# Kernel optimization log

Measured on AMD Instinct MI355X. Metric: run time of the kernel, lower is better.

Reference implementation:

```python
import jax, jax.numpy as jnp
import numpy as np

PI_APPROX = 3.1415926  # the source uses 3.1415926, not math.pi
N_RINGS = 10
N_ANGLES = 36  # k in range(0, 360, 10)


def setup_inputs() -> dict:
    key = jax.random.key(0)
    k1, k2, k3 = jax.random.split(key, 3)
    B, N = 32, 16384
    pred = jax.random.normal(k1, (B, N_RINGS), dtype=jnp.float32)
    target = jax.random.normal(k2, (B, N, 3), dtype=jnp.float32)
    trans_feat = jax.random.normal(k3, (B, 256), dtype=jnp.float32)
    return {"pred": pred, "target": target, "trans_feat": trans_feat}


def _generate_points(pred):
    # pred: [B, 10] radii. For ring j: center = [0.04, 0.15*j - 0.7, 0.0],
    # axis = y, firstPoint (centered) = [-r, 0, 0]. Rotating about y by angle a:
    # R @ [-r,0,0] = [-r*cos(a), 0, r*sin(a)]; then add center back.
    B = pred.shape[0]
    j = jnp.arange(N_RINGS, dtype=pred.dtype)
    cy = 0.15 * j - 0.7                                   # [10]
    ang = jnp.arange(0, 360, 10, dtype=pred.dtype) * (2.0 * PI_APPROX / 360.0)  # [36]
    c, s = jnp.cos(ang), jnp.sin(ang)
    r = pred[:, :, None]                                  # [B,10,1]
    px = -r * c[None, None, :] + 0.04                     # [B,10,36]
    py = jnp.broadcast_to(cy[None, :, None], px.shape)    # [B,10,36]
    pz = r * s[None, None, :]                             # [B,10,36]
    pts = jnp.stack([px, py, pz], axis=-1)                # [B,10,36,3]
    return pts.reshape(B, N_RINGS * N_ANGLES, 3)          # [B,360,3]


def reference(pred, target, trans_feat):
    B = pred.shape[0]
    pts = _generate_points(pred.reshape(B, N_RINGS))      # [B,360,3]
    # squared pairwise distances via ||a||^2 + ||b||^2 - 2 a.b
    d2 = (jnp.sum(pts * pts, axis=-1)[:, :, None]
          + jnp.sum(target * target, axis=-1)[:, None, :]
          - 2.0 * jnp.einsum('bpd,bnd->bpn', pts, target))  # [B,360,N]
    d2 = jnp.maximum(d2, 0.0)
    # original: min over target of ||pt - tgt||, then squared == min of squared dist
    min_d2 = jnp.min(d2, axis=-1)                         # [B,360]
    return jnp.mean(min_d2)
```

## Files before the change

kernel.cpp:

```cpp
#include <hip/hip_runtime.h>
#include <math.h>
#include <float.h>

#define N_RINGS  10
#define N_ANGLES 36
#define NP       (N_RINGS * N_ANGLES)
#define PI_APPROX 3.1415926f

#define BLOCK  256
#define WPB    4
#define CHUNK  1024
#define NPAIR  (CHUNK / 2)
#define PPT    6

typedef float f2 __attribute__((ext_vector_type(2)));

__global__ __launch_bounds__(BLOCK) void chamfer_minbuf(
    const float* __restrict__ pred,
    const float* __restrict__ target,
    unsigned int* __restrict__ minbuf,
    int N, int chunks)
{
    __shared__ float4 txy[NPAIR];
    __shared__ float4 tzw[NPAIR];
    __shared__ float  pm[WPB * NP];
    __shared__ float  cs_c[N_ANGLES], cs_s[N_ANGLES];

    const int b   = blockIdx.x / chunks;
    const int cg  = blockIdx.x % chunks;
    const int n0  = cg * CHUNK;
    const int tid = threadIdx.x;
    const int cnt = min(CHUNK, N - n0);
    const int npairs = (cnt + 1) >> 1;

    if (tid < N_ANGLES) {
        float angf = (float)(10 * tid) * (2.0f * PI_APPROX / 360.0f);
        double ang = (double)angf;
        cs_c[tid] = (float)cos(ang);
        cs_s[tid] = (float)sin(ang);
    }
    for (int p = tid; p < npairs; p += BLOCK) {
        const int i0 = 2 * p;
        const int i1 = min(2 * p + 1, cnt - 1);
        const float* t0 = target + ((size_t)b * N + (size_t)(n0 + i0)) * 3;
        const float* t1 = target + ((size_t)b * N + (size_t)(n0 + i1)) * 3;
        float x0 = t0[0], y0 = t0[1], z0 = t0[2];
        float x1 = t1[0], y1 = t1[1], z1 = t1[2];
        float w0 = x0 * x0 + y0 * y0 + z0 * z0;
        float w1 = x1 * x1 + y1 * y1 + z1 * z1;
        txy[p] = make_float4(x0, x1, y0, y1);
        tzw[p] = make_float4(z0, z1, w0, w1);
    }
    __syncthreads();

    const int lane = tid & 63;
    const int w    = tid >> 6;

    f2 qx2[PPT], qy2[PPT], qz2[PPT], m2[PPT];
    float pp2[PPT];
    #pragma unroll
    for (int k = 0; k < PPT; ++k) {
        int s = lane + 64 * k;
        int j = s / N_ANGLES;
        int a = s - j * N_ANGLES;
        int jc = (j < N_RINGS) ? j : (N_RINGS - 1);
        float r  = pred[b * N_RINGS + jc];
        float px = -r * cs_c[a] + 0.04f;
        float py = 0.15f * (float)jc - 0.7f;
        float pz = r * cs_s[a];
        pp2[k] = px * px + py * py + pz * pz;
        float qxv = -2.0f * px, qyv = -2.0f * py, qzv = -2.0f * pz;
        qx2[k] = (f2){qxv, qxv};
        qy2[k] = (f2){qyv, qyv};
        qz2[k] = (f2){qzv, qzv};
        m2[k]  = (f2){FLT_MAX, FLT_MAX};
    }

    #pragma unroll 4
    for (int k = w; k < npairs; k += WPB) {
        float4 A  = txy[k];
        float4 Bz = tzw[k];
        f2 X  = {A.x,  A.y };
        f2 Y  = {A.z,  A.w };
        f2 Z  = {Bz.x, Bz.y};
        f2 W2 = {Bz.z, Bz.w};
        #pragma unroll
        for (int i = 0; i < PPT; ++i) {
            f2 h = __builtin_elementwise_fma(qz2[i], Z, W2);
            h = __builtin_elementwise_fma(qy2[i], Y, h);
            h = __builtin_elementwise_fma(qx2[i], X, h);
            m2[i] = __builtin_elementwise_min(m2[i], h);
        }
    }

    #pragma unroll
    for (int k = 0; k < PPT; ++k) {
        int s = lane + 64 * k;
        if (s < NP) {
            float mv = fminf(m2[k].x, m2[k].y);
            pm[w * NP + s] = fmaxf(pp2[k] + mv, 0.0f);
        }
    }
    __syncthreads();

    for (int p = tid; p < NP; p += BLOCK) {
        float v = fminf(fminf(pm[p], pm[NP + p]),
                        fminf(pm[2 * NP + p], pm[3 * NP + p]));
        atomicMin(&minbuf[b * NP + p], __float_as_uint(v));
    }
}

__global__ __launch_bounds__(1024) void reduce_mean(
    const unsigned int* __restrict__ minbuf, float* __restrict__ out,
    int count)
{
    __shared__ double sm[16];
    const int tid = threadIdx.x;
    double s = 0.0;
    const int n4 = count >> 2;
    const uint4* v4 = (const uint4*)minbuf;
    for (int i = tid; i < n4; i += 1024) {
        uint4 u = v4[i];
        s += (double)__uint_as_float(u.x) + (double)__uint_as_float(u.y)
           + (double)__uint_as_float(u.z) + (double)__uint_as_float(u.w);
    }
    for (int i = 4 * n4 + tid; i < count; i += 1024)
        s += (double)__uint_as_float(minbuf[i]);
    #pragma unroll
    for (int off = 32; off > 0; off >>= 1)
        s += __shfl_down(s, off, 64);
    if ((tid & 63) == 0) sm[tid >> 6] = s;
    __syncthreads();
    if (tid == 0) {
        double tot = 0.0;
        for (int wv = 0; wv < 16; ++wv) tot += sm[wv];
        out[0] = (float)(tot / (double)count);
    }
}

extern "C" void kernel_launch(void* const* d_in, const int* in_sizes, int n_in,
                              void* d_out, int out_size, void* d_ws, size_t ws_size,
                              hipStream_t stream) {
    const float* pred   = (const float*)d_in[0];
    const float* target = (const float*)d_in[1];

    const int B = in_sizes[0] / N_RINGS;
    const int N = in_sizes[1] / (3 * B);
    const int chunks = (N + CHUNK - 1) / CHUNK;
    const int count  = B * NP;

    unsigned int* minbuf = (unsigned int*)d_ws;
    float* out = (float*)d_out;

    hipMemsetAsync(minbuf, 0xFF, (size_t)count * sizeof(unsigned int), stream);

    hipLaunchKernelGGL(chamfer_minbuf, dim3(B * chunks), dim3(BLOCK), 0, stream,
                       pred, target, minbuf, N, chunks);
    hipLaunchKernelGGL(reduce_mean, dim3(1), dim3(1024), 0, stream,
                       minbuf, out, count);
}
```

Baseline: 81.45 us.

## Fuse mean reduction into chamfer kernel via last-block ticket and double block size

Removes the separate single-block reduce kernel by having each block take a ticket from an atomic counter placed after the min buffer. The last block to finish sums the min buffer and writes the mean. The counter is initialised to 0xFFFFFFFF by the memset, which is why the last block is detected as gridDim-2. The block size also grows to 512 threads with 8 waves splitting the target chunk, which cuts per-wave loop length but adds an 8-way min merge. This saves a kernel launch at the cost of a fence and atomic in every block, plus a serial tail done by a 512-thread block.

```diff
diff --git a/kernel.cpp b/kernel.cpp
--- a/kernel.cpp
+++ b/kernel.cpp
@@ -7,24 +7,27 @@
 #define NP       (N_RINGS * N_ANGLES)
 #define PI_APPROX 3.1415926f
 
-#define BLOCK  256
-#define WPB    4
+#define BLOCK  512
+#define WPB    8
 #define CHUNK  1024
 #define NPAIR  (CHUNK / 2)
 #define PPT    6
 
 typedef float f2 __attribute__((ext_vector_type(2)));
 
-__global__ __launch_bounds__(BLOCK) void chamfer_minbuf(
+__global__ __launch_bounds__(BLOCK, 4) void chamfer_fused(
     const float* __restrict__ pred,
     const float* __restrict__ target,
     unsigned int* __restrict__ minbuf,
-    int N, int chunks)
+    float* __restrict__ out,
+    int N, int chunks, int count)
 {
     __shared__ float4 txy[NPAIR];
     __shared__ float4 tzw[NPAIR];
     __shared__ float  pm[WPB * NP];
     __shared__ float  cs_c[N_ANGLES], cs_s[N_ANGLES];
+    __shared__ unsigned int ticket;
+    __shared__ double sm[WPB];
 
     const int b   = blockIdx.x / chunks;
     const int cg  = blockIdx.x % chunks;
@@ -104,37 +107,36 @@
     __syncthreads();
 
     for (int p = tid; p < NP; p += BLOCK) {
-        float v = fminf(fminf(pm[p], pm[NP + p]),
-                        fminf(pm[2 * NP + p], pm[3 * NP + p]));
+        float v = pm[p];
+        #pragma unroll
+        for (int wv = 1; wv < WPB; ++wv)
+            v = fminf(v, pm[wv * NP + p]);
         atomicMin(&minbuf[b * NP + p], __float_as_uint(v));
     }
-}
 
-__global__ __launch_bounds__(1024) void reduce_mean(
-    const unsigned int* __restrict__ minbuf, float* __restrict__ out,
-    int count)
-{
-    __shared__ double sm[16];
-    const int tid = threadIdx.x;
-    double s = 0.0;
-    const int n4 = count >> 2;
-    const uint4* v4 = (const uint4*)minbuf;
-    for (int i = tid; i < n4; i += 1024) {
-        uint4 u = v4[i];
-        s += (double)__uint_as_float(u.x) + (double)__uint_as_float(u.y)
-           + (double)__uint_as_float(u.z) + (double)__uint_as_float(u.w);
-    }
-    for (int i = 4 * n4 + tid; i < count; i += 1024)
-        s += (double)__uint_as_float(minbuf[i]);
-    #pragma unroll
-    for (int off = 32; off > 0; off >>= 1)
-        s += __shfl_down(s, off, 64);
-    if ((tid & 63) == 0) sm[tid >> 6] = s;
+    __threadfence();
+    if (tid == 0)
+        ticket = atomicAdd(&minbuf[count], 1u);
     __syncthreads();
-    if (tid == 0) {
-        double tot = 0.0;
-        for (int wv = 0; wv < 16; ++wv) tot += sm[wv];
-        out[0] = (float)(tot / (double)count);
+    if (ticket == (unsigned int)gridDim.x - 2u) {
+        __threadfence();
+        double s = 0.0;
+        for (int i = tid; i < count; i += BLOCK) {
+            unsigned int u = __hip_atomic_load(&minbuf[i], __ATOMIC_RELAXED,
+                                               __HIP_MEMORY_SCOPE_AGENT);
+            s += (double)__uint_as_float(u);
+        }
+        #pragma unroll
+        for (int off = 32; off > 0; off >>= 1)
+            s += __shfl_down(s, off, 64);
+        if (lane == 0) sm[w] = s;
+        __syncthreads();
+        if (tid == 0) {
+            double tot = 0.0;
+            #pragma unroll
+            for (int wv = 0; wv < WPB; ++wv) tot += sm[wv];
+            out[0] = (float)(tot / (double)count);
+        }
     }
 }
 
@@ -152,10 +154,9 @@
     unsigned int* minbuf = (unsigned int*)d_ws;
     float* out = (float*)d_out;
 
-    hipMemsetAsync(minbuf, 0xFF, (size_t)count * sizeof(unsigned int), stream);
+    hipMemsetAsync(minbuf, 0xFF, ((size_t)count + 1) * sizeof(unsigned int),
+                   stream);
 
-    hipLaunchKernelGGL(chamfer_minbuf, dim3(B * chunks), dim3(BLOCK), 0, stream,
-                       pred, target, minbuf, N, chunks);
-    hipLaunchKernelGGL(reduce_mean, dim3(1), dim3(1024), 0, stream,
-                       minbuf, out, count);
+    hipLaunchKernelGGL(chamfer_fused, dim3(B * chunks), dim3(BLOCK), 0, stream,
+                       pred, target, minbuf, out, N, chunks, count);
 }
```

Result: slower. 140.4 us (+72.4%).
